# Kernel tuning notes

Hardware: AMD Instinct MI355X
Metric: run time of the kernel (lower is better)

## Reference

```python
import jax, jax.numpy as jnp
import numpy as np

PAD_IDX = 1
B, L, E, H = 2, 256, 512, 8
D = E // H
SCALE = D ** -0.5


def setup_inputs() -> dict:
    key = jax.random.key(0)
    ks = jax.random.split(key, 10)
    std = 0.02
    return {
        "queries": jax.random.normal(ks[0], (B, L, E), jnp.float32),
        "keys": jax.random.normal(ks[1], (B, L, E), jnp.float32),
        "values": jax.random.normal(ks[2], (B, L, E), jnp.float32),
        "relation": jax.random.normal(ks[3], (B, L, L, E), jnp.float32),
        "adj_mask": jax.random.randint(ks[4], (B, L, L), 0, 2, jnp.int32),
        "Wq": jax.random.normal(ks[5], (E, E), jnp.float32) * std,
        "bq": jnp.zeros((E,), jnp.float32),
        "Wk": jax.random.normal(ks[6], (E, E), jnp.float32) * std,
        "bk": jnp.zeros((E,), jnp.float32),
        "Wv": jax.random.normal(ks[7], (E, E), jnp.float32) * std,
        "bv": jnp.zeros((E,), jnp.float32),
        "Wr": jax.random.normal(ks[8], (2 * E, E), jnp.float32) * std,
        "Wo": jax.random.normal(ks[9], (E, E), jnp.float32) * std,
        "bo": jnp.zeros((E,), jnp.float32),
    }


def reference(queries, keys, values, relation, adj_mask,
              Wq, bq, Wk, bk, Wv, bv, Wr, Wo, bo):
    b, t, _ = queries.shape
    s = keys.shape[1]
    # input projections (torch Linear: y = x @ W.T + b)
    q = ((queries @ Wq.T + bq) * SCALE).reshape(b, t, H, D)
    k = (keys @ Wk.T + bk).reshape(b, s, H, D)
    v = (values @ Wv.T + bv).reshape(b, s, H, D)
    # relation projection -> relation queries/keys, [b, t, s, H, D] then transpose(1,2)
    rel = relation @ Wr.T                              # [b, t, s, 2E]
    rq, rk = jnp.split(rel, 2, axis=-1)
    rq = rq.reshape(b, t, s, H, D).transpose(0, 2, 1, 3, 4)  # [b, s, t, H, D]
    rk = rk.reshape(b, t, s, H, D).transpose(0, 2, 1, 3, 4)
    # broadcasted relation bias (requires t == s, as in the original)
    qe = q[:, :, None] + rq                            # [b, t, s, H, D]
    ke = k[:, None] + rk                               # [b, t, s, H, D]
    attn = jnp.einsum('bijhn,bijhn->bijh', qe, ke)     # [b, t, s, H]
    pad = (adj_mask == PAD_IDX)[..., None]             # [b, t, s, 1]
    attn = jnp.where(pad, -jnp.inf, attn)
    attn_weights = jax.nn.softmax(attn, axis=2)
    out = jnp.einsum('bijh,bjhn->bihn', attn_weights, v).reshape(b, t, E)
    out = out @ Wo.T + bo
    return out, attn_weights
```

## Files before the change

kernel.cpp:

```cpp
#include <hip/hip_runtime.h>

typedef unsigned int uint32;
typedef __attribute__((ext_vector_type(8))) short bf16x8;
typedef __attribute__((ext_vector_type(4))) float f32x4;


__device__ __forceinline__ uint32 bf_rne(uint32 u) {
  return (u + 0x7fffu + ((u >> 16) & 1u)) >> 16;
}

__global__ void cvt_wr_kernel(const float* __restrict__ Wr, unsigned short* __restrict__ WrBf) {
  int idx = blockIdx.x * 256 + threadIdx.x;
  const uint4* src = (const uint4*)Wr;
  uint4 x = src[idx];
  uint2 o;
  o.x = bf_rne(x.x) | (bf_rne(x.y) << 16);
  o.y = bf_rne(x.z) | (bf_rne(x.w) << 16);
  ((uint2*)WrBf)[idx] = o;
}

__global__ __launch_bounds__(256) void proj_kernel(
    const float* __restrict__ X0, const float* __restrict__ W0, const float* __restrict__ b0, float* __restrict__ Y0,
    const float* __restrict__ X1, const float* __restrict__ W1, const float* __restrict__ b1, float* __restrict__ Y1,
    const float* __restrict__ X2, const float* __restrict__ W2, const float* __restrict__ b2, float* __restrict__ Y2,
    float scale0) {
  int z = blockIdx.z;
  const float* X = (z == 0) ? X0 : (z == 1) ? X1 : X2;
  const float* W = (z == 0) ? W0 : (z == 1) ? W1 : W2;
  const float* bias = (z == 0) ? b0 : (z == 1) ? b1 : b2;
  float* Y = (z == 0) ? Y0 : (z == 1) ? Y1 : Y2;
  float scale = (z == 0) ? scale0 : 1.0f;

  __shared__ float Xs[16][68];
  __shared__ float Ws[16][68];

  int tid = threadIdx.x;
  int tx = tid & 15, ty = tid >> 4;
  int m0 = blockIdx.x * 64, n0 = blockIdx.y * 64;

  float acc[4][4] = {};

  for (int k0 = 0; k0 < 512; k0 += 16) {
#pragma unroll
    for (int u = 0; u < 4; ++u) {
      int idx = tid + u * 256;
      int ml = idx >> 4, kl = idx & 15;
      Xs[kl][ml] = X[(size_t)(m0 + ml) * 512 + k0 + kl];
      Ws[kl][ml] = W[(size_t)(n0 + ml) * 512 + k0 + kl];
    }
    __syncthreads();
#pragma unroll
    for (int kk = 0; kk < 16; ++kk) {
      float4 a = *(const float4*)&Xs[kk][ty * 4];
      float4 w = *(const float4*)&Ws[kk][tx * 4];
      float av[4] = {a.x, a.y, a.z, a.w};
      float wv[4] = {w.x, w.y, w.z, w.w};
#pragma unroll
      for (int i = 0; i < 4; ++i)
#pragma unroll
        for (int jj = 0; jj < 4; ++jj)
          acc[i][jj] += av[i] * wv[jj];
    }
    __syncthreads();
  }
#pragma unroll
  for (int i = 0; i < 4; ++i) {
    int m = m0 + ty * 4 + i;
#pragma unroll
    for (int jj = 0; jj < 4; ++jj) {
      int n = n0 + tx * 4 + jj;
      Y[(size_t)m * 512 + n] = (acc[i][jj] + bias[n]) * scale;
    }
  }
}

__global__ __launch_bounds__(256, 3) void rel_score_kernel(
    const float* __restrict__ rel,
    const unsigned short* __restrict__ wrbf,
    const float* __restrict__ qws,
    const float* __restrict__ kws,
    float* __restrict__ attn)
{
  __shared__ unsigned short As[2][64 * 72];
  __shared__ float scores[4][64];

  const int tid = threadIdx.x;
  const int lane = tid & 63;
  const int wv = tid >> 6;
  const int blk = blockIdx.x;
  const int hp = blk & 3;
  const int mt = blk >> 2;
  const int b = mt >> 10;
  const int j = (mt >> 2) & 255;
  const int i0 = (mt & 3) << 6;
  const int h0 = hp << 1;

  const float* Abase = rel + (size_t)mt * (64 * 512);

  const int t15 = lane & 15;
  const int kq = (lane >> 4) * 8;

  const unsigned short* bptr[4];
#pragma unroll
  for (int fc = 0; fc < 4; ++fc) {
    int g = (wv & 1) * 4 + fc;
    int wr_row = (g & 1) * 512 + (h0 + (wv >> 1)) * 64 + (g >> 1) * 16 + t15;
    bptr[fc] = wrbf + (size_t)wr_row * 512 + kq;
  }

  const int arow0 = tid >> 3;
  const int ak8 = (tid & 7) * 8;
  const uint4* aptr0 = (const uint4*)(Abase + (size_t)arow0 * 512 + ak8);
  const uint4* aptr1 = (const uint4*)(Abase + (size_t)(arow0 + 32) * 512 + ak8);

  f32x4 acc[4][4];
#pragma unroll
  for (int a = 0; a < 4; ++a)
#pragma unroll
    for (int c = 0; c < 4; ++c)
      acc[a][c] = (f32x4){0.f, 0.f, 0.f, 0.f};

  uint4 p0 = aptr0[0];
  uint4 p1 = aptr0[1];
  uint4 p2 = aptr1[0];
  uint4 p3 = aptr1[1];

  for (int k = 0; k < 8; ++k) {
    const int k0 = k * 64;
    bf16x8 bfr[2][4];
#pragma unroll
    for (int kh = 0; kh < 2; ++kh)
#pragma unroll
      for (int fc = 0; fc < 4; ++fc)
        bfr[kh][fc] = *(const bf16x8*)(bptr[fc] + k0 + kh * 32);
    unsigned short* asb = As[k & 1];
    {
      uint4 o;
      o.x = (p0.y & 0xffff0000u) | (p0.x >> 16);
      o.y = (p0.w & 0xffff0000u) | (p0.z >> 16);
      o.z = (p1.y & 0xffff0000u) | (p1.x >> 16);
      o.w = (p1.w & 0xffff0000u) | (p1.z >> 16);
      *(uint4*)&asb[arow0 * 72 + ak8] = o;
      o.x = (p2.y & 0xffff0000u) | (p2.x >> 16);
      o.y = (p2.w & 0xffff0000u) | (p2.z >> 16);
      o.z = (p3.y & 0xffff0000u) | (p3.x >> 16);
      o.w = (p3.w & 0xffff0000u) | (p3.z >> 16);
      *(uint4*)&asb[(arow0 + 32) * 72 + ak8] = o;
    }
    if (k < 7) {
      const uint4* n0p = (const uint4*)((const float*)aptr0 + (k + 1) * 64);
      const uint4* n1p = (const uint4*)((const float*)aptr1 + (k + 1) * 64);
      p0 = n0p[0];
      p1 = n0p[1];
      p2 = n1p[0];
      p3 = n1p[1];
    }
    __syncthreads();
#pragma unroll
    for (int kh = 0; kh < 2; ++kh) {
      int kk = kh * 32 + kq;
      bf16x8 af[4];
#pragma unroll
      for (int fr = 0; fr < 4; ++fr)
        af[fr] = *(const bf16x8*)&asb[(fr * 16 + t15) * 72 + kk];
#pragma unroll
      for (int fr = 0; fr < 4; ++fr)
#pragma unroll
        for (int fc = 0; fc < 4; ++fc)
          acc[fr][fc] = __builtin_amdgcn_mfma_f32_16x16x32_bf16(
              af[fr], bfr[kh][fc], acc[fr][fc], 0, 0, 0);
    }
  }

  const int hthis = h0 + (wv >> 1);
  const int dbase = (wv & 1) * 32;
  const float* qbase = qws + ((size_t)(b * 256 + i0)) * 512 + hthis * 64;
  const float* krow = kws + ((size_t)(b * 256 + j)) * 512 + hthis * 64;
  const int rgrp = lane >> 4;
#pragma unroll
  for (int fr = 0; fr < 4; ++fr) {
#pragma unroll
    for (int r = 0; r < 4; ++r) {
      int m = fr * 16 + rgrp * 4 + r;
      float s = 0.f;
#pragma unroll
      for (int p = 0; p < 2; ++p) {
        int d = dbase + p * 16 + t15;
        float qv = qbase[(size_t)m * 512 + d];
        float kv = krow[d];
        s += (qv + acc[fr][p * 2][r]) * (kv + acc[fr][p * 2 + 1][r]);
      }
      s += __shfl_xor(s, 1);
      s += __shfl_xor(s, 2);
      s += __shfl_xor(s, 4);
      s += __shfl_xor(s, 8);
      if (t15 == 0) scores[wv][m] = s;
    }
  }
  __syncthreads();
  if (tid < 128) {
    int hl = tid >> 6, m = tid & 63;
    float sc = scores[hl * 2][m] + scores[hl * 2 + 1][m];
    attn[(((size_t)(b * 256 + i0 + m)) * 256 + j) * 8 + (h0 + hl)] = sc;
  }
}

__global__ __launch_bounds__(256) void softmax_av_kernel(
    float* __restrict__ attn, const int* __restrict__ adj,
    const float* __restrict__ vws, float* __restrict__ o1) {
  __shared__ float sl[2048];
  __shared__ int msk[256];
  int bi = blockIdx.x;
  int b = bi >> 8;
  float* base = attn + (size_t)bi * 2048;
  const int* abase = adj + (size_t)bi * 256;
  int tid = threadIdx.x;
#pragma unroll
  for (int u = 0; u < 8; ++u) sl[tid + u * 256] = base[tid + u * 256];
  msk[tid] = abase[tid];
  __syncthreads();
  int h = tid >> 5, l5 = tid & 31;
  float mx = -INFINITY;
#pragma unroll
  for (int u = 0; u < 8; ++u) {
    int jj = l5 + u * 32;
    if (msk[jj] != 1) mx = fmaxf(mx, sl[jj * 8 + h]);
  }
#pragma unroll
  for (int off = 16; off >= 1; off >>= 1) mx = fmaxf(mx, __shfl_xor(mx, off));
  float ev[8];
  float sum = 0.f;
#pragma unroll
  for (int u = 0; u < 8; ++u) {
    int jj = l5 + u * 32;
    float e = (msk[jj] != 1) ? __expf(sl[jj * 8 + h] - mx) : 0.f;
    ev[u] = e;
    sum += e;
  }
#pragma unroll
  for (int off = 16; off >= 1; off >>= 1) sum += __shfl_xor(sum, off);
  float inv = (sum > 0.f) ? (1.f / sum) : 0.f;
#pragma unroll
  for (int u = 0; u < 8; ++u) {
    int jj = l5 + u * 32;
    sl[jj * 8 + h] = ev[u] * inv;
  }
  __syncthreads();
#pragma unroll
  for (int u = 0; u < 8; ++u) base[tid + u * 256] = sl[tid + u * 256];
  const float* vbase = vws + (size_t)b * (256 * 512);
  int e0 = tid, e1 = tid + 256;
  int h0 = e0 >> 6, h1 = e1 >> 6;
  float a0 = 0.f, a1 = 0.f;
  for (int jj = 0; jj < 256; ++jj) {
    float w0 = sl[jj * 8 + h0];
    float w1 = sl[jj * 8 + h1];
    const float* vr = vbase + (size_t)jj * 512;
    a0 += w0 * vr[e0];
    a1 += w1 * vr[e1];
  }
  float* orow = o1 + (size_t)bi * 512;
  orow[e0] = a0;
  orow[e1] = a1;
}

extern "C" void kernel_launch(void* const* d_in, const int* in_sizes, int n_in,
                              void* d_out, int out_size, void* d_ws, size_t ws_size,
                              hipStream_t stream) {
  const float* queries = (const float*)d_in[0];
  const float* keys    = (const float*)d_in[1];
  const float* values  = (const float*)d_in[2];
  const float* relation = (const float*)d_in[3];
  const int*   adj     = (const int*)d_in[4];
  const float* Wq = (const float*)d_in[5];
  const float* bq = (const float*)d_in[6];
  const float* Wk = (const float*)d_in[7];
  const float* bk = (const float*)d_in[8];
  const float* Wv = (const float*)d_in[9];
  const float* bv = (const float*)d_in[10];
  const float* Wr = (const float*)d_in[11];
  const float* Wo = (const float*)d_in[12];
  const float* bo = (const float*)d_in[13];

  float* out  = (float*)d_out;
  float* attn = out + 262144;

  float* ws  = (float*)d_ws;
  float* qws = ws;
  float* kws = ws + 262144;
  float* vws = ws + 524288;
  float* o1  = ws + 786432;
  unsigned short* wrbf = (unsigned short*)(ws + 1048576);

  cvt_wr_kernel<<<dim3(512), dim3(256), 0, stream>>>(Wr, wrbf);

  proj_kernel<<<dim3(8, 8, 3), dim3(256), 0, stream>>>(
      queries, Wq, bq, qws,
      keys,    Wk, bk, kws,
      values,  Wv, bv, vws,
      0.125f);

  rel_score_kernel<<<dim3(8192), dim3(256), 0, stream>>>(relation, wrbf, qws, kws, attn);

  softmax_av_kernel<<<dim3(512), dim3(256), 0, stream>>>(attn, adj, vws, o1);

  proj_kernel<<<dim3(8, 8, 1), dim3(256), 0, stream>>>(
      o1, Wo, bo, out,
      nullptr, nullptr, nullptr, nullptr,
      nullptr, nullptr, nullptr, nullptr,
      1.0f);
}
```

Before: 697.0 us.

## Reuse relation tile in LDS across all head pairs within one block

Each block now converts its full 64x512 relation tile to bf16 once, keeps the whole K extent in shared memory, and loops over the four head pairs, running the MFMA GEMM and score epilogue per pair. Previously four separate blocks each re-read the same fp32 relation tile from global memory, one per head pair. The aim is to cut the dominant global read traffic about fourfold. In exchange, shared memory per block grows substantially, occupancy drops (launch bounds lowered to 2), and per-block work is serialized across head pairs.

```diff
diff --git a/kernel.cpp b/kernel.cpp
--- a/kernel.cpp
+++ b/kernel.cpp
@@ -74,26 +74,23 @@
   }
 }
 
-__global__ __launch_bounds__(256, 3) void rel_score_kernel(
+__global__ __launch_bounds__(256, 2) void rel_score_kernel(
     const float* __restrict__ rel,
     const unsigned short* __restrict__ wrbf,
     const float* __restrict__ qws,
     const float* __restrict__ kws,
     float* __restrict__ attn)
 {
-  __shared__ unsigned short As[2][64 * 72];
-  __shared__ float scores[4][64];
+  __shared__ unsigned short As[64 * 520];
+  __shared__ float scores[4][4][64];
 
   const int tid = threadIdx.x;
   const int lane = tid & 63;
   const int wv = tid >> 6;
-  const int blk = blockIdx.x;
-  const int hp = blk & 3;
-  const int mt = blk >> 2;
+  const int mt = blockIdx.x;
   const int b = mt >> 10;
   const int j = (mt >> 2) & 255;
   const int i0 = (mt & 3) << 6;
-  const int h0 = hp << 1;
 
   const float* Abase = rel + (size_t)mt * (64 * 512);
 
@@ -104,7 +101,7 @@
 #pragma unroll
   for (int fc = 0; fc < 4; ++fc) {
     int g = (wv & 1) * 4 + fc;
-    int wr_row = (g & 1) * 512 + (h0 + (wv >> 1)) * 64 + (g >> 1) * 16 + t15;
+    int wr_row = (g & 1) * 512 + (wv >> 1) * 64 + (g >> 1) * 16 + t15;
     bptr[fc] = wrbf + (size_t)wr_row * 512 + kq;
   }
 
@@ -114,6 +111,41 @@
   const uint4* aptr1 = (const uint4*)(Abase + (size_t)(arow0 + 32) * 512 + ak8);
 
   f32x4 acc[4][4];
+
+  auto epilogue = [&](int hp) {
+    const int hthis = hp * 2 + (wv >> 1);
+    const int dbase = (wv & 1) * 32;
+    const float* qbase = qws + ((size_t)(b * 256 + i0)) * 512 + hthis * 64;
+    const float* krow = kws + ((size_t)(b * 256 + j)) * 512 + hthis * 64;
+    const int rgrp = lane >> 4;
+#pragma unroll
+    for (int fr = 0; fr < 4; ++fr) {
+#pragma unroll
+      for (int r = 0; r < 4; ++r) {
+        int m = fr * 16 + rgrp * 4 + r;
+        float s = 0.f;
+#pragma unroll
+        for (int p = 0; p < 2; ++p) {
+          int d = dbase + p * 16 + t15;
+          float qv = qbase[(size_t)m * 512 + d];
+          float kv = krow[d];
+          s += (qv + acc[fr][p * 2][r]) * (kv + acc[fr][p * 2 + 1][r]);
+        }
+        s += __shfl_xor(s, 1);
+        s += __shfl_xor(s, 2);
+        s += __shfl_xor(s, 4);
+        s += __shfl_xor(s, 8);
+        if (t15 == 0) scores[hp][wv][m] = s;
+      }
+    }
+    __syncthreads();
+    if (tid < 128) {
+      int hl = tid >> 6, m = tid & 63;
+      float sc = scores[hp][hl * 2][m] + scores[hp][hl * 2 + 1][m];
+      attn[(((size_t)(b * 256 + i0 + m)) * 256 + j) * 8 + hp * 2 + hl] = sc;
+    }
+  };
+
 #pragma unroll
   for (int a = 0; a < 4; ++a)
 #pragma unroll
@@ -133,19 +165,18 @@
 #pragma unroll
       for (int fc = 0; fc < 4; ++fc)
         bfr[kh][fc] = *(const bf16x8*)(bptr[fc] + k0 + kh * 32);
-    unsigned short* asb = As[k & 1];
     {
       uint4 o;
       o.x = (p0.y & 0xffff0000u) | (p0.x >> 16);
       o.y = (p0.w & 0xffff0000u) | (p0.z >> 16);
       o.z = (p1.y & 0xffff0000u) | (p1.x >> 16);
       o.w = (p1.w & 0xffff0000u) | (p1.z >> 16);
-      *(uint4*)&asb[arow0 * 72 + ak8] = o;
+      *(uint4*)&As[arow0 * 520 + k0 + ak8] = o;
       o.x = (p2.y & 0xffff0000u) | (p2.x >> 16);
       o.y = (p2.w & 0xffff0000u) | (p2.z >> 16);
       o.z = (p3.y & 0xffff0000u) | (p3.x >> 16);
       o.w = (p3.w & 0xffff0000u) | (p3.z >> 16);
-      *(uint4*)&asb[(arow0 + 32) * 72 + ak8] = o;
+      *(uint4*)&As[(arow0 + 32) * 520 + k0 + ak8] = o;
     }
     if (k < 7) {
       const uint4* n0p = (const uint4*)((const float*)aptr0 + (k + 1) * 64);
@@ -158,11 +189,11 @@
     __syncthreads();
 #pragma unroll
     for (int kh = 0; kh < 2; ++kh) {
-      int kk = kh * 32 + kq;
+      int kk = k0 + kh * 32 + kq;
       bf16x8 af[4];
 #pragma unroll
       for (int fr = 0; fr < 4; ++fr)
-        af[fr] = *(const bf16x8*)&asb[(fr * 16 + t15) * 72 + kk];
+        af[fr] = *(const bf16x8*)&As[(fr * 16 + t15) * 520 + kk];
 #pragma unroll
       for (int fr = 0; fr < 4; ++fr)
 #pragma unroll
@@ -171,37 +202,58 @@
               af[fr], bfr[kh][fc], acc[fr][fc], 0, 0, 0);
     }
   }
-
-  const int hthis = h0 + (wv >> 1);
-  const int dbase = (wv & 1) * 32;
-  const float* qbase = qws + ((size_t)(b * 256 + i0)) * 512 + hthis * 64;
-  const float* krow = kws + ((size_t)(b * 256 + j)) * 512 + hthis * 64;
-  const int rgrp = lane >> 4;
-#pragma unroll
-  for (int fr = 0; fr < 4; ++fr) {
-#pragma unroll
-    for (int r = 0; r < 4; ++r) {
-      int m = fr * 16 + rgrp * 4 + r;
-      float s = 0.f;
-#pragma unroll
-      for (int p = 0; p < 2; ++p) {
-        int d = dbase + p * 16 + t15;
-        float qv = qbase[(size_t)m * 512 + d];
-        float kv = krow[d];
-        s += (qv + acc[fr][p * 2][r]) * (kv + acc[fr][p * 2 + 1][r]);
+  epilogue(0);
+
+  for (int hp = 1; hp < 4; ++hp) {
+#pragma unroll
+    for (int a = 0; a < 4; ++a)
+#pragma unroll
+      for (int c = 0; c < 4; ++c)
+        acc[a][c] = (f32x4){0.f, 0.f, 0.f, 0.f};
+
+    const int hofs = hp * 65536;
+
+    bf16x8 bfr[2][4];
+#pragma unroll
+    for (int kh = 0; kh < 2; ++kh)
+#pragma unroll
+      for (int fc = 0; fc < 4; ++fc)
+        bfr[kh][fc] = *(const bf16x8*)(bptr[fc] + hofs + kh * 32);
+
+#pragma unroll
+    for (int k = 0; k < 8; ++k) {
+      const int k0 = k * 64;
+      bf16x8 bnx[2][4];
+      if (k < 7) {
+#pragma unroll
+        for (int kh = 0; kh < 2; ++kh)
+#pragma unroll
+          for (int fc = 0; fc < 4; ++fc)
+            bnx[kh][fc] = *(const bf16x8*)(bptr[fc] + hofs + k0 + 64 + kh * 32);
       }
-      s += __shfl_xor(s, 1);
-      s += __shfl_xor(s, 2);
-      s += __shfl_xor(s, 4);
-      s += __shfl_xor(s, 8);
-      if (t15 == 0) scores[wv][m] = s;
-    }
-  }
-  __syncthreads();
-  if (tid < 128) {
-    int hl = tid >> 6, m = tid & 63;
-    float sc = scores[hl * 2][m] + scores[hl * 2 + 1][m];
-    attn[(((size_t)(b * 256 + i0 + m)) * 256 + j) * 8 + (h0 + hl)] = sc;
+#pragma unroll
+      for (int kh = 0; kh < 2; ++kh) {
+        int kk = k0 + kh * 32 + kq;
+        bf16x8 af[4];
+#pragma unroll
+        for (int fr = 0; fr < 4; ++fr)
+          af[fr] = *(const bf16x8*)&As[(fr * 16 + t15) * 520 + kk];
+#pragma unroll
+        for (int fr = 0; fr < 4; ++fr)
+#pragma unroll
+          for (int fc = 0; fc < 4; ++fc)
+            acc[fr][fc] = __builtin_amdgcn_mfma_f32_16x16x32_bf16(
+                af[fr], bfr[kh][fc], acc[fr][fc], 0, 0, 0);
+      }
+      if (k < 7) {
+#pragma unroll
+        for (int kh = 0; kh < 2; ++kh)
+#pragma unroll
+          for (int fc = 0; fc < 4; ++fc)
+            bfr[kh][fc] = bnx[kh][fc];
+      }
+    }
+    epilogue(hp);
   }
 }
 
@@ -300,7 +352,7 @@
       values,  Wv, bv, vws,
       0.125f);
 
-  rel_score_kernel<<<dim3(8192), dim3(256), 0, stream>>>(relation, wrbf, qws, kws, attn);
+  rel_score_kernel<<<dim3(2048), dim3(256), 0, stream>>>(relation, wrbf, qws, kws, attn);
 
   softmax_av_kernel<<<dim3(512), dim3(256), 0, stream>>>(attn, adj, vws, o1);
 
```

New measurement: 738.3 us. 5.9% more time.
